# Performance work log

Hardware: AMD Instinct MI355X
Metric: run time of the kernel (lower is better)

## Reference

```python
import jax, jax.numpy as jnp
import numpy as np

B, W, M, HD, RL, RD = 32, 32, 1024, 64, 2, 32
D = RL * HD  # concat of per-layer hidden states


def setup_inputs() -> dict:
    key = jax.random.key(0)
    ks = jax.random.split(key, 16)
    s = 0.1
    r = lambda k, shape: (jax.random.normal(k, shape, jnp.float32) * s)
    return {
        "x_input": jax.random.normal(ks[0], (B, W, M), jnp.float32),
        "major_graph": jax.random.normal(ks[1], (M, M), jnp.float32) * 0.02,
        "H_init": jnp.zeros((RL, M, HD), jnp.float32),
        # GRU layer 0: input size 1 -> hidden HD
        "Wih0": r(ks[2], (3 * HD, 1)),
        "Whh0": r(ks[3], (3 * HD, HD)),
        "bih0": jnp.zeros((3 * HD,), jnp.float32),
        "bhh0": jnp.zeros((3 * HD,), jnp.float32),
        # GRU layer 1: hidden HD -> hidden HD
        "Wih1": r(ks[4], (3 * HD, HD)),
        "Whh1": r(ks[5], (3 * HD, HD)),
        "bih1": jnp.zeros((3 * HD,), jnp.float32),
        "bhh1": jnp.zeros((3 * HD,), jnp.float32),
        # weight-normed Linear(RL*HD -> RD)
        "V": r(ks[6], (RD, D)),
        "g": jnp.ones((RD,), jnp.float32),
        "b_lin": jnp.zeros((RD,), jnp.float32),
        # FinalRowWise layer: per-node weights [M, RD] -> scalar per node
        "W_fr": r(ks[7], (M, RD)),
        "b_fr": jnp.zeros((M,), jnp.float32),
    }


def _gru_cell(x, h, Wih, Whh, bih, bhh):
    # x: [B, M, in], h: [B, M, HD]
    gi = x @ Wih.T + bih
    gh = h @ Whh.T + bhh
    ir, iz, inn = jnp.split(gi, 3, axis=-1)
    hr, hz, hnn = jnp.split(gh, 3, axis=-1)
    rgate = jax.nn.sigmoid(ir + hr)
    zgate = jax.nn.sigmoid(iz + hz)
    n = jnp.tanh(inn + rgate * hnn)
    return (1.0 - zgate) * n + zgate * h


def reference(x_input, major_graph, H_init, Wih0, Whh0, bih0, bhh0,
              Wih1, Whh1, bih1, bhh1, V, g, b_lin, W_fr, b_fr):
    Bn, Wn_, Mn = x_input.shape
    # h0: [RL, B, M, HD] (H_init broadcast over batch)
    h0 = jnp.broadcast_to(H_init[:, None], (H_init.shape[0], Bn, Mn, H_init.shape[-1]))
    # weight_norm (dim=0): per-output-row normalization of V scaled by g
    Wn = g[:, None] * V / jnp.linalg.norm(V, axis=1, keepdims=True)  # [RD, D]
    x_seq = jnp.transpose(x_input, (1, 0, 2))[..., None]  # [W, B, M, 1]

    def step(hn, x_t):
        hn0 = _gru_cell(x_t, hn, Wih0, Whh0, bih0, bhh0)        # [B, M, HD]
        hn1 = _gru_cell(hn0, h0[1], Wih1, Whh1, bih1, bhh1)     # [B, M, HD] (fresh h0 each step, as in source)
        x_p = jnp.concatenate([hn0, hn1], axis=-1)              # [B, M, D]
        # graph-weighted projection along node axis: x_p @ major_graph
        x_g = jax.nn.relu(jnp.einsum('bid,ij->bjd', x_p, major_graph))  # [B, M, D]
        y = jax.nn.sigmoid(x_g @ Wn.T + b_lin)                  # [B, M, RD]
        out = jnp.einsum('bmd,md->bm', y, W_fr) + b_fr          # [B, M]
        return hn1, out

    _, outs = jax.lax.scan(step, h0[0], x_seq)  # [W, B, M]
    return jnp.transpose(outs, (1, 0, 2))       # [B, W, M]
```

## Files before the change

### kernel.cpp

```cpp
#include <hip/hip_runtime.h>
#include <math.h>

#define B_  32
#define W_  32
#define M_  1024
#define HD_ 64
#define RD_ 32
#define D_  128
#define CH_ 16
#define NKT 16

typedef short bf16x8 __attribute__((ext_vector_type(8)));
typedef float f32x4  __attribute__((ext_vector_type(4)));

#define AS1 __attribute__((address_space(1)))
#define AS3 __attribute__((address_space(3)))

__device__ __forceinline__ void gload16(const void* g, void* l) {
    __builtin_amdgcn_global_load_lds((const AS1 void*)g, (AS3 void*)l, 16, 0, 0);
}

__device__ __forceinline__ void bar_lds() {
    asm volatile("s_waitcnt lgkmcnt(0)" ::: "memory");
    __builtin_amdgcn_s_barrier();
    asm volatile("" ::: "memory");
}

__device__ __forceinline__ unsigned short f2b(float f) {
    unsigned int u = __float_as_uint(f);
    u += 0x7fffu + ((u >> 16) & 1u);
    return (unsigned short)(u >> 16);
}
__device__ __forceinline__ float b2f(unsigned short h) {
    return __uint_as_float(((unsigned int)h) << 16);
}
__device__ __forceinline__ float sigf(float x) { return 1.0f / (1.0f + __expf(-x)); }
__device__ __forceinline__ float tanhf_(float x) { return 2.0f / (1.0f + __expf(-2.0f * x)) - 1.0f; }


__global__ __launch_bounds__(256) void gt_kernel(const float* __restrict__ G,
                                                 unsigned short* __restrict__ GTb) {
    __shared__ float T[64][65];
    int i0 = blockIdx.x * 64, j0 = blockIdx.y * 64;
    int tid = threadIdx.x;
    int r = tid >> 4, c4 = (tid & 15) * 4;
    #pragma unroll
    for (int q = 0; q < 4; ++q) {
        float4 v = *(const float4*)&G[(i0 + r + q * 16) * M_ + j0 + c4];
        T[r + q * 16][c4] = v.x; T[r + q * 16][c4 + 1] = v.y;
        T[r + q * 16][c4 + 2] = v.z; T[r + q * 16][c4 + 3] = v.w;
    }
    __syncthreads();
    #pragma unroll
    for (int q = 0; q < 4; ++q) {
        int jr = r + q * 16;
        ushort4 o;
        o.x = f2b(T[c4][jr]); o.y = f2b(T[c4 + 1][jr]);
        o.z = f2b(T[c4 + 2][jr]); o.w = f2b(T[c4 + 3][jr]);
        *(ushort4*)&GTb[(j0 + jr) * M_ + i0 + c4] = o;
    }
}

__global__ __launch_bounds__(192) void gh1ct_kernel(const float* __restrict__ H_init,
                                                    const float* __restrict__ Whh1,
                                                    const float* __restrict__ bhh1,
                                                    float* __restrict__ gh1cT) {
    int m = blockIdx.x, k = threadIdx.x;
    __shared__ float h01[HD_];
    if (k < HD_) h01[k] = H_init[(M_ + m) * HD_ + k];
    __syncthreads();
    float d = 0.f;
    #pragma unroll
    for (int hd = 0; hd < HD_; ++hd) d = fmaf(h01[hd], Whh1[k * HD_ + hd], d);
    gh1cT[k * M_ + m] = d + bhh1[k];
}

__global__ __launch_bounds__(128) void wn_kernel(const float* __restrict__ V,
                                                 const float* __restrict__ g,
                                                 unsigned short* __restrict__ Wnb) {
    int r = blockIdx.x, d = threadIdx.x;
    float v = V[r * D_ + d];
    float s = v * v;
    #pragma unroll
    for (int off = 32; off > 0; off >>= 1) s += __shfl_down(s, off);
    __shared__ float ws[2];
    if ((threadIdx.x & 63) == 0) ws[threadIdx.x >> 6] = s;
    __syncthreads();
    float norm = sqrtf(ws[0] + ws[1]);
    Wnb[r * D_ + d] = f2b(g[r] * v / norm);
}

__global__ __launch_bounds__(256) void castw_kernel(const float* __restrict__ Whh0,
                                                    const float* __restrict__ Wih1,
                                                    unsigned short* __restrict__ Whh0b,
                                                    unsigned short* __restrict__ Wih1b) {
    int i = blockIdx.x * 256 + threadIdx.x;
    Whh0b[i] = f2b(Whh0[i]);
    Wih1b[i] = f2b(Wih1[i]);
}

__global__ __launch_bounds__(256) void inith_kernel(const float* __restrict__ H_init,
                                                    unsigned short* __restrict__ Hb) {
    int e8 = blockIdx.x * 256 + threadIdx.x;
    int base = e8 * 8;
    int src = base & (M_ * HD_ - 1);
    float4 v0 = *(const float4*)&H_init[src];
    float4 v1 = *(const float4*)&H_init[src + 4];
    uint4 u;
    u.x = (unsigned int)f2b(v0.x) | ((unsigned int)f2b(v0.y) << 16);
    u.y = (unsigned int)f2b(v0.z) | ((unsigned int)f2b(v0.w) << 16);
    u.z = (unsigned int)f2b(v1.x) | ((unsigned int)f2b(v1.y) << 16);
    u.w = (unsigned int)f2b(v1.z) | ((unsigned int)f2b(v1.w) << 16);
    *(uint4*)&Hb[base] = u;
}

__global__ __launch_bounds__(512, 4) void gru_chunk_kernel(
    const float* __restrict__ x_input, const float* __restrict__ Wih0,
    const float* __restrict__ bih0, const float* __restrict__ bhh0,
    const unsigned short* __restrict__ Whh0b, const unsigned short* __restrict__ Wih1b,
    const float* __restrict__ bih1, const float* __restrict__ gh1cT,
    const float* __restrict__ H_init, unsigned short* __restrict__ Hb,
    unsigned short* __restrict__ XPT_c, int t0)
{
    __shared__ unsigned short Whh0s[192 * 64];
    __shared__ unsigned short Wih1s[192 * 64];
    __shared__ unsigned short hn0s[64 * 64];
    __shared__ unsigned short hn1s[64 * 64];
    const int tid = threadIdx.x, w = tid >> 6, l = tid & 63;
    const int li = l & 15, lh = l >> 4;
    const int pg = w >> 1, hf = w & 1;
    const int b = blockIdx.x >> 4, mt = blockIdx.x & 15;
    const int m0 = mt * 64;
    const int p0b = b * M_ + m0;
    const int ms = m0 + pg * 16;

    for (int i = tid; i < 1536; i += 512) {
        int row = i >> 3, pos = i & 7, sc = pos ^ (row & 7);
        gload16(&Whh0b[row * 64 + sc * 8], (char*)Whh0s + (i & ~63) * 16);
        gload16(&Wih1b[row * 64 + sc * 8], (char*)Wih1s + (i & ~63) * 16);
    }
    {
        int p = tid >> 3, cc = tid & 7;
        uint4 v = *(const uint4*)&Hb[(p0b + p) * HD_ + cc * 8];
        *(uint4*)((char*)hn1s + p * 128 + ((cc ^ (p & 7)) << 4)) = v;
    }

    float wi_[3][2], bi0_[3][2], bh0_[3][2], bi1_[3][2];
    float vrA[2][4], vzA[2][4], vnA[2][4], h01A[2][4];
    #pragma unroll
    for (int fi = 0; fi < 2; ++fi) {
        int ko = hf * 32 + fi * 16 + li;
        #pragma unroll
        for (int g3 = 0; g3 < 3; ++g3) {
            wi_[g3][fi]  = Wih0[g3 * 64 + ko];
            bi0_[g3][fi] = bih0[g3 * 64 + ko];
            bh0_[g3][fi] = bhh0[g3 * 64 + ko];
            bi1_[g3][fi] = bih1[g3 * 64 + ko];
        }
        float4 vr = *(const float4*)&gh1cT[(ko) * M_ + ms + lh * 4];
        float4 vz = *(const float4*)&gh1cT[(64 + ko) * M_ + ms + lh * 4];
        float4 vn = *(const float4*)&gh1cT[(128 + ko) * M_ + ms + lh * 4];
        vrA[fi][0] = vr.x; vrA[fi][1] = vr.y; vrA[fi][2] = vr.z; vrA[fi][3] = vr.w;
        vzA[fi][0] = vz.x; vzA[fi][1] = vz.y; vzA[fi][2] = vz.z; vzA[fi][3] = vz.w;
        vnA[fi][0] = vn.x; vnA[fi][1] = vn.y; vnA[fi][2] = vn.z; vnA[fi][3] = vn.w;
        #pragma unroll
        for (int reg = 0; reg < 4; ++reg)
            h01A[fi][reg] = H_init[M_ * HD_ + (ms + lh * 4 + reg) * HD_ + ko];
    }

    asm volatile("s_waitcnt vmcnt(0) lgkmcnt(0)" ::: "memory");
    __builtin_amdgcn_s_barrier();
    asm volatile("" ::: "memory");

    float hst[2][4];
    #pragma unroll
    for (int fi = 0; fi < 2; ++fi) {
        int ko = hf * 32 + fi * 16 + li;
        #pragma unroll
        for (int reg = 0; reg < 4; ++reg) {
            int ml = pg * 16 + lh * 4 + reg;
            hst[fi][reg] = b2f(*(const unsigned short*)((char*)hn1s + ml * 128 +
                               ((((ko >> 3) ^ (ml & 7))) << 4) + (ko & 7) * 2));
        }
    }

    for (int ts = 0; ts < CH_; ++ts) {
        int t = t0 + ts;
        float4 xv = *(const float4*)&x_input[(b * W_ + t) * M_ + ms + lh * 4];
        float x4[4] = {xv.x, xv.y, xv.z, xv.w};
        const int rl = pg * 16 + li;

        bf16x8 a0 = *(const bf16x8*)((char*)hn1s + rl * 128 + ((lh ^ (rl & 7)) << 4));
        bf16x8 a1 = *(const bf16x8*)((char*)hn1s + rl * 128 + (((4 + lh) ^ (rl & 7)) << 4));
        f32x4 acc[6];
        #pragma unroll
        for (int q = 0; q < 6; ++q) acc[q] = (f32x4){0.f, 0.f, 0.f, 0.f};
        #pragma unroll
        for (int g3 = 0; g3 < 3; ++g3)
            #pragma unroll
            for (int fi = 0; fi < 2; ++fi) {
                int row = (g3 * 4 + hf * 2 + fi) * 16 + li;
                bf16x8 b0 = *(const bf16x8*)((char*)Whh0s + row * 128 + ((lh ^ (row & 7)) << 4));
                bf16x8 b1 = *(const bf16x8*)((char*)Whh0s + row * 128 + (((4 + lh) ^ (row & 7)) << 4));
                acc[g3 * 2 + fi] = __builtin_amdgcn_mfma_f32_16x16x32_bf16(a0, b0, acc[g3 * 2 + fi], 0, 0, 0);
                acc[g3 * 2 + fi] = __builtin_amdgcn_mfma_f32_16x16x32_bf16(a1, b1, acc[g3 * 2 + fi], 0, 0, 0);
            }
        #pragma unroll
        for (int fi = 0; fi < 2; ++fi) {
            int j = hf * 32 + fi * 16 + li;
            #pragma unroll
            for (int reg = 0; reg < 4; ++reg) {
                int ml = pg * 16 + lh * 4 + reg;
                float x = x4[reg];
                float r = sigf(x * wi_[0][fi] + bi0_[0][fi] + acc[fi][reg]     + bh0_[0][fi]);
                float z = sigf(x * wi_[1][fi] + bi0_[1][fi] + acc[2 + fi][reg] + bh0_[1][fi]);
                float n = tanhf_(x * wi_[2][fi] + bi0_[2][fi] + r * (acc[4 + fi][reg] + bh0_[2][fi]));
                float h0v = (1.f - z) * n + z * hst[fi][reg];
                *(unsigned short*)((char*)hn0s + ml * 128 +
                    ((((j >> 3) ^ (ml & 7))) << 4) + (j & 7) * 2) = f2b(h0v);
            }
        }
        bar_lds();

        a0 = *(const bf16x8*)((char*)hn0s + rl * 128 + ((lh ^ (rl & 7)) << 4));
        a1 = *(const bf16x8*)((char*)hn0s + rl * 128 + (((4 + lh) ^ (rl & 7)) << 4));
        #pragma unroll
        for (int q = 0; q < 6; ++q) acc[q] = (f32x4){0.f, 0.f, 0.f, 0.f};
        #pragma unroll
        for (int g3 = 0; g3 < 3; ++g3)
            #pragma unroll
            for (int fi = 0; fi < 2; ++fi) {
                int row = (g3 * 4 + hf * 2 + fi) * 16 + li;
                bf16x8 b0 = *(const bf16x8*)((char*)Wih1s + row * 128 + ((lh ^ (row & 7)) << 4));
                bf16x8 b1 = *(const bf16x8*)((char*)Wih1s + row * 128 + (((4 + lh) ^ (row & 7)) << 4));
                acc[g3 * 2 + fi] = __builtin_amdgcn_mfma_f32_16x16x32_bf16(a0, b0, acc[g3 * 2 + fi], 0, 0, 0);
                acc[g3 * 2 + fi] = __builtin_amdgcn_mfma_f32_16x16x32_bf16(a1, b1, acc[g3 * 2 + fi], 0, 0, 0);
            }
        #pragma unroll
        for (int fi = 0; fi < 2; ++fi) {
            int ko = hf * 32 + fi * 16 + li;
            #pragma unroll
            for (int reg = 0; reg < 4; ++reg) {
                int ml = pg * 16 + lh * 4 + reg;
                float r = sigf(acc[fi][reg]     + bi1_[0][fi] + vrA[fi][reg]);
                float z = sigf(acc[2 + fi][reg] + bi1_[1][fi] + vzA[fi][reg]);
                float n = tanhf_(acc[4 + fi][reg] + bi1_[2][fi] + r * vnA[fi][reg]);
                float h1v = (1.f - z) * n + z * h01A[fi][reg];
                hst[fi][reg] = h1v;
                *(unsigned short*)((char*)hn1s + ml * 128 +
                    ((((ko >> 3) ^ (ml & 7))) << 4) + (ko & 7) * 2) = f2b(h1v);
            }
        }
        bar_lds();

        {
            unsigned short* XPT = XPT_c + (size_t)ts * (D_ * B_ * M_);
            int d = tid >> 2, mh = (tid & 3) * 16;
            const char* src = (d < 64) ? (const char*)hn0s : (const char*)hn1s;
            int dd = d & 63;
            unsigned int pk[8];
            #pragma unroll
            for (int mm = 0; mm < 16; mm += 2) {
                int ma = mh + mm, mb = mh + mm + 1;
                unsigned int ua = *(const unsigned short*)(src + ma * 128 + (((dd >> 3) ^ (ma & 7)) << 4) + (dd & 7) * 2);
                unsigned int ub = *(const unsigned short*)(src + mb * 128 + (((dd >> 3) ^ (mb & 7)) << 4) + (dd & 7) * 2);
                pk[mm >> 1] = ua | (ub << 16);
            }
            uint4 o0 = {pk[0], pk[1], pk[2], pk[3]};
            uint4 o1 = {pk[4], pk[5], pk[6], pk[7]};
            *(uint4*)&XPT[(b * D_ + d) * M_ + m0 + mh]     = o0;
            *(uint4*)&XPT[(b * D_ + d) * M_ + m0 + mh + 8] = o1;
        }
        bar_lds();
    }

    {
        int p = tid >> 3, cc = tid & 7;
        uint4 v = *(const uint4*)((char*)hn1s + p * 128 + ((cc ^ (p & 7)) << 4));
        *(uint4*)&Hb[(p0b + p) * HD_ + cc * 8] = v;
    }
}

__global__ __launch_bounds__(512, 4) void gemmhead_kernel(
    const unsigned short* __restrict__ GTb, const unsigned short* __restrict__ XPT_c,
    const unsigned short* __restrict__ Wnb, const float* __restrict__ b_lin,
    const float* __restrict__ W_fr, const float* __restrict__ b_fr,
    float* __restrict__ out, int t0)
{
    __shared__ __align__(16) char lds[65536];
    const int tid = threadIdx.x, w = tid >> 6, l = tid & 63;
    const int li = l & 15, lh = l >> 4;
    const int wm = w >> 2, wn = w & 3;
    const int bid = blockIdx.x;
    const int ntile = (bid & 7) + ((bid >> 6) << 3);
    const int j0 = ((bid >> 3) & 7) * 128;
    const unsigned short* Asrc = GTb + (size_t)j0 * M_;
    const unsigned short* Bsrc = XPT_c + (size_t)ntile * 128 * M_;

    f32x4 acc[4][2];
    #pragma unroll
    for (int mi = 0; mi < 4; ++mi)
        #pragma unroll
        for (int ni = 0; ni < 2; ++ni) acc[mi][ni] = (f32x4){0.f, 0.f, 0.f, 0.f};

    #define STAGE(kt, c) { \
        _Pragma("unroll") \
        for (int q = 0; q < 2; ++q) { \
            int i = q * 512 + tid; \
            int row = i >> 3, pos = i & 7, sc = pos ^ (row & 7); \
            gload16(&Asrc[row * M_ + (kt) * 64 + sc * 8], lds + (c) * 32768 + (i & ~63) * 16); \
            gload16(&Bsrc[row * M_ + (kt) * 64 + sc * 8], lds + (c) * 32768 + 16384 + (i & ~63) * 16); \
        } }

    STAGE(0, 0);

    for (int kt = 0; kt < NKT; ++kt) {
        if (kt + 1 < NKT) { STAGE(kt + 1, (kt + 1) & 1);
                            asm volatile("s_waitcnt vmcnt(4)" ::: "memory"); }
        else              { asm volatile("s_waitcnt vmcnt(0)" ::: "memory"); }
        __builtin_amdgcn_s_barrier();
        asm volatile("" ::: "memory");
        const char* Abuf = lds + (kt & 1) * 32768;
        const char* Bbuf = Abuf + 16384;
        bf16x8 af[4][2], bfv[2][2];
        #pragma unroll
        for (int mi = 0; mi < 4; ++mi) {
            int row = wm * 64 + mi * 16 + li;
            #pragma unroll
            for (int kk = 0; kk < 2; ++kk)
                af[mi][kk] = *(const bf16x8*)(Abuf + row * 128 + (((kk * 4 + lh) ^ (row & 7)) << 4));
        }
        #pragma unroll
        for (int ni = 0; ni < 2; ++ni) {
            int row = wn * 32 + ni * 16 + li;
            #pragma unroll
            for (int kk = 0; kk < 2; ++kk)
                bfv[ni][kk] = *(const bf16x8*)(Bbuf + row * 128 + (((kk * 4 + lh) ^ (row & 7)) << 4));
        }
        __builtin_amdgcn_s_setprio(1);
        #pragma unroll
        for (int kk = 0; kk < 2; ++kk)
            #pragma unroll
            for (int mi = 0; mi < 4; ++mi)
                #pragma unroll
                for (int ni = 0; ni < 2; ++ni)
                    acc[mi][ni] = __builtin_amdgcn_mfma_f32_16x16x32_bf16(af[mi][kk], bfv[ni][kk], acc[mi][ni], 0, 0, 0);
        __builtin_amdgcn_s_setprio(0);
        asm volatile("s_waitcnt lgkmcnt(0)" ::: "memory");
        __builtin_amdgcn_s_barrier();
        asm volatile("" ::: "memory");
    }

    __syncthreads();

    #pragma unroll
    for (int mi = 0; mi < 4; ++mi)
        #pragma unroll
        for (int ni = 0; ni < 2; ++ni)
            #pragma unroll
            for (int reg = 0; reg < 4; ++reg) {
                int jl = wm * 64 + mi * 16 + lh * 4 + reg;
                int cl = wn * 32 + ni * 16 + li;
                float v = fmaxf(acc[mi][ni][reg], 0.f);
                int byte = jl * 256 + ((((cl >> 3) ^ (jl & 7))) << 4) + (cl & 7) * 2;
                *(unsigned short*)(lds + byte) = f2b(v);
            }
    __syncthreads();

    const int b = ntile & 31, t = t0 + (ntile >> 5);
    float bl0 = b_lin[li], bl1 = b_lin[16 + li];
    {
        int row = w * 16 + li;
        f32x4 P0 = (f32x4){0.f, 0.f, 0.f, 0.f};
        f32x4 P1 = (f32x4){0.f, 0.f, 0.f, 0.f};
        #pragma unroll
        for (int ks = 0; ks < 4; ++ks) {
            int cp = (ks * 4 + lh) ^ (row & 7);
            bf16x8 xa = *(const bf16x8*)(lds + row * 256 + cp * 16);
            bf16x8 wb0 = *(const bf16x8*)&Wnb[(li) * D_ + ks * 32 + lh * 8];
            bf16x8 wb1 = *(const bf16x8*)&Wnb[(16 + li) * D_ + ks * 32 + lh * 8];
            P0 = __builtin_amdgcn_mfma_f32_16x16x32_bf16(xa, wb0, P0, 0, 0, 0);
            P1 = __builtin_amdgcn_mfma_f32_16x16x32_bf16(xa, wb1, P1, 0, 0, 0);
        }
        float s[4];
        #pragma unroll
        for (int reg = 0; reg < 4; ++reg) {
            int j = j0 + w * 16 + lh * 4 + reg;
            float y0 = sigf(P0[reg] + bl0);
            float y1 = sigf(P1[reg] + bl1);
            s[reg] = y0 * W_fr[j * RD_ + li] + y1 * W_fr[j * RD_ + 16 + li];
        }
        #pragma unroll
        for (int off = 1; off < 16; off <<= 1) {
            #pragma unroll
            for (int reg = 0; reg < 4; ++reg) s[reg] += __shfl_xor(s[reg], off);
        }
        if (li == 0) {
            int jb = j0 + w * 16 + lh * 4;
            float4 o = {s[0] + b_fr[jb], s[1] + b_fr[jb + 1],
                        s[2] + b_fr[jb + 2], s[3] + b_fr[jb + 3]};
            *(float4*)&out[(b * W_ + t) * M_ + jb] = o;
        }
    }
}


extern "C" void kernel_launch(void* const* d_in, const int* in_sizes, int n_in,
                              void* d_out, int out_size, void* d_ws, size_t ws_size,
                              hipStream_t stream) {
    const float* x_input = (const float*)d_in[0];
    const float* G       = (const float*)d_in[1];
    const float* H_init  = (const float*)d_in[2];
    const float* Wih0    = (const float*)d_in[3];
    const float* Whh0    = (const float*)d_in[4];
    const float* bih0    = (const float*)d_in[5];
    const float* bhh0    = (const float*)d_in[6];
    const float* Wih1    = (const float*)d_in[7];
    const float* Whh1    = (const float*)d_in[8];
    const float* bih1    = (const float*)d_in[9];
    const float* bhh1    = (const float*)d_in[10];
    const float* V       = (const float*)d_in[11];
    const float* gvec    = (const float*)d_in[12];
    const float* b_lin   = (const float*)d_in[13];
    const float* W_fr    = (const float*)d_in[14];
    const float* b_fr    = (const float*)d_in[15];
    float* out = (float*)d_out;

    char* ws = (char*)d_ws;
    unsigned short* GTb   = (unsigned short*)(ws);
    unsigned short* XPT_c = (unsigned short*)(ws + (2u   << 20));
    unsigned short* Hb    = (unsigned short*)(ws + (130u << 20));
    float*          gh1cT = (float*)(ws + (134u << 20));
    unsigned short* Wnb   = (unsigned short*)(ws + (135u << 20));
    unsigned short* Whh0b = (unsigned short*)(ws + (135u << 20) + 8192);
    unsigned short* Wih1b = (unsigned short*)(ws + (135u << 20) + 8192 + 24576);

    gt_kernel   <<<dim3(16, 16), 256, 0, stream>>>(G, GTb);
    gh1ct_kernel<<<M_, 192, 0, stream>>>(H_init, Whh1, bhh1, gh1cT);
    wn_kernel   <<<RD_, 128, 0, stream>>>(V, gvec, Wnb);
    castw_kernel<<<48, 256, 0, stream>>>(Whh0, Wih1, Whh0b, Wih1b);
    inith_kernel<<<1024, 256, 0, stream>>>(H_init, Hb);

    for (int c = 0; c < W_ / CH_; ++c) {
        gru_chunk_kernel<<<512, 512, 0, stream>>>(x_input, Wih0, bih0, bhh0, Whh0b,
                                                  Wih1b, bih1, gh1cT, H_init, Hb,
                                                  XPT_c, c * CH_);
        gemmhead_kernel<<<dim3(4096), 512, 0, stream>>>(GTb, XPT_c, Wnb, b_lin,
                                                        W_fr, b_fr, out, c * CH_);
    }
}
```

Before: 584.5 us.

## Double GRU chunk block to 1024 threads, one hidden quarter per wave

```diff
diff --git a/kernel.cpp b/kernel.cpp
--- a/kernel.cpp
+++ b/kernel.cpp
@@ -114,7 +114,7 @@
     *(uint4*)&Hb[base] = u;
 }
 
-__global__ __launch_bounds__(512, 4) void gru_chunk_kernel(
+__global__ __launch_bounds__(1024, 8) void gru_chunk_kernel(
     const float* __restrict__ x_input, const float* __restrict__ Wih0,
     const float* __restrict__ bih0, const float* __restrict__ bhh0,
     const unsigned short* __restrict__ Whh0b, const unsigned short* __restrict__ Wih1b,
@@ -128,60 +128,55 @@
     __shared__ unsigned short hn1s[64 * 64];
     const int tid = threadIdx.x, w = tid >> 6, l = tid & 63;
     const int li = l & 15, lh = l >> 4;
-    const int pg = w >> 1, hf = w & 1;
+    const int pg = w >> 2, qf = w & 3;
     const int b = blockIdx.x >> 4, mt = blockIdx.x & 15;
     const int m0 = mt * 64;
     const int p0b = b * M_ + m0;
     const int ms = m0 + pg * 16;
 
-    for (int i = tid; i < 1536; i += 512) {
+    for (int i = tid; i < 1536; i += 1024) {
         int row = i >> 3, pos = i & 7, sc = pos ^ (row & 7);
         gload16(&Whh0b[row * 64 + sc * 8], (char*)Whh0s + (i & ~63) * 16);
         gload16(&Wih1b[row * 64 + sc * 8], (char*)Wih1s + (i & ~63) * 16);
     }
-    {
+    if (tid < 512) {
         int p = tid >> 3, cc = tid & 7;
         uint4 v = *(const uint4*)&Hb[(p0b + p) * HD_ + cc * 8];
         *(uint4*)((char*)hn1s + p * 128 + ((cc ^ (p & 7)) << 4)) = v;
     }
 
-    float wi_[3][2], bi0_[3][2], bh0_[3][2], bi1_[3][2];
-    float vrA[2][4], vzA[2][4], vnA[2][4], h01A[2][4];
-    #pragma unroll
-    for (int fi = 0; fi < 2; ++fi) {
-        int ko = hf * 32 + fi * 16 + li;
-        #pragma unroll
-        for (int g3 = 0; g3 < 3; ++g3) {
-            wi_[g3][fi]  = Wih0[g3 * 64 + ko];
-            bi0_[g3][fi] = bih0[g3 * 64 + ko];
-            bh0_[g3][fi] = bhh0[g3 * 64 + ko];
-            bi1_[g3][fi] = bih1[g3 * 64 + ko];
-        }
+    const int ko = qf * 16 + li;
+    float wi_[3], bi0_[3], bh0_[3], bi1_[3];
+    #pragma unroll
+    for (int g3 = 0; g3 < 3; ++g3) {
+        wi_[g3]  = Wih0[g3 * 64 + ko];
+        bi0_[g3] = bih0[g3 * 64 + ko];
+        bh0_[g3] = bhh0[g3 * 64 + ko];
+        bi1_[g3] = bih1[g3 * 64 + ko];
+    }
+    float vrA[4], vzA[4], vnA[4], h01A[4];
+    {
         float4 vr = *(const float4*)&gh1cT[(ko) * M_ + ms + lh * 4];
         float4 vz = *(const float4*)&gh1cT[(64 + ko) * M_ + ms + lh * 4];
         float4 vn = *(const float4*)&gh1cT[(128 + ko) * M_ + ms + lh * 4];
-        vrA[fi][0] = vr.x; vrA[fi][1] = vr.y; vrA[fi][2] = vr.z; vrA[fi][3] = vr.w;
-        vzA[fi][0] = vz.x; vzA[fi][1] = vz.y; vzA[fi][2] = vz.z; vzA[fi][3] = vz.w;
-        vnA[fi][0] = vn.x; vnA[fi][1] = vn.y; vnA[fi][2] = vn.z; vnA[fi][3] = vn.w;
+        vrA[0] = vr.x; vrA[1] = vr.y; vrA[2] = vr.z; vrA[3] = vr.w;
+        vzA[0] = vz.x; vzA[1] = vz.y; vzA[2] = vz.z; vzA[3] = vz.w;
+        vnA[0] = vn.x; vnA[1] = vn.y; vnA[2] = vn.z; vnA[3] = vn.w;
         #pragma unroll
         for (int reg = 0; reg < 4; ++reg)
-            h01A[fi][reg] = H_init[M_ * HD_ + (ms + lh * 4 + reg) * HD_ + ko];
+            h01A[reg] = H_init[M_ * HD_ + (ms + lh * 4 + reg) * HD_ + ko];
     }
 
     asm volatile("s_waitcnt vmcnt(0) lgkmcnt(0)" ::: "memory");
     __builtin_amdgcn_s_barrier();
     asm volatile("" ::: "memory");
 
-    float hst[2][4];
-    #pragma unroll
-    for (int fi = 0; fi < 2; ++fi) {
-        int ko = hf * 32 + fi * 16 + li;
-        #pragma unroll
-        for (int reg = 0; reg < 4; ++reg) {
-            int ml = pg * 16 + lh * 4 + reg;
-            hst[fi][reg] = b2f(*(const unsigned short*)((char*)hn1s + ml * 128 +
-                               ((((ko >> 3) ^ (ml & 7))) << 4) + (ko & 7) * 2));
-        }
+    float hst[4];
+    #pragma unroll
+    for (int reg = 0; reg < 4; ++reg) {
+        int ml = pg * 16 + lh * 4 + reg;
+        hst[reg] = b2f(*(const unsigned short*)((char*)hn1s + ml * 128 +
+                       ((((ko >> 3) ^ (ml & 7))) << 4) + (ko & 7) * 2));
     }
 
     for (int ts = 0; ts < CH_; ++ts) {
@@ -192,89 +187,75 @@
 
         bf16x8 a0 = *(const bf16x8*)((char*)hn1s + rl * 128 + ((lh ^ (rl & 7)) << 4));
         bf16x8 a1 = *(const bf16x8*)((char*)hn1s + rl * 128 + (((4 + lh) ^ (rl & 7)) << 4));
-        f32x4 acc[6];
-        #pragma unroll
-        for (int q = 0; q < 6; ++q) acc[q] = (f32x4){0.f, 0.f, 0.f, 0.f};
-        #pragma unroll
-        for (int g3 = 0; g3 < 3; ++g3)
-            #pragma unroll
-            for (int fi = 0; fi < 2; ++fi) {
-                int row = (g3 * 4 + hf * 2 + fi) * 16 + li;
-                bf16x8 b0 = *(const bf16x8*)((char*)Whh0s + row * 128 + ((lh ^ (row & 7)) << 4));
-                bf16x8 b1 = *(const bf16x8*)((char*)Whh0s + row * 128 + (((4 + lh) ^ (row & 7)) << 4));
-                acc[g3 * 2 + fi] = __builtin_amdgcn_mfma_f32_16x16x32_bf16(a0, b0, acc[g3 * 2 + fi], 0, 0, 0);
-                acc[g3 * 2 + fi] = __builtin_amdgcn_mfma_f32_16x16x32_bf16(a1, b1, acc[g3 * 2 + fi], 0, 0, 0);
-            }
-        #pragma unroll
-        for (int fi = 0; fi < 2; ++fi) {
-            int j = hf * 32 + fi * 16 + li;
-            #pragma unroll
-            for (int reg = 0; reg < 4; ++reg) {
-                int ml = pg * 16 + lh * 4 + reg;
-                float x = x4[reg];
-                float r = sigf(x * wi_[0][fi] + bi0_[0][fi] + acc[fi][reg]     + bh0_[0][fi]);
-                float z = sigf(x * wi_[1][fi] + bi0_[1][fi] + acc[2 + fi][reg] + bh0_[1][fi]);
-                float n = tanhf_(x * wi_[2][fi] + bi0_[2][fi] + r * (acc[4 + fi][reg] + bh0_[2][fi]));
-                float h0v = (1.f - z) * n + z * hst[fi][reg];
-                *(unsigned short*)((char*)hn0s + ml * 128 +
-                    ((((j >> 3) ^ (ml & 7))) << 4) + (j & 7) * 2) = f2b(h0v);
-            }
+        f32x4 acc[3];
+        #pragma unroll
+        for (int q = 0; q < 3; ++q) acc[q] = (f32x4){0.f, 0.f, 0.f, 0.f};
+        #pragma unroll
+        for (int g3 = 0; g3 < 3; ++g3) {
+            int row = (g3 * 4 + qf) * 16 + li;
+            bf16x8 b0 = *(const bf16x8*)((char*)Whh0s + row * 128 + ((lh ^ (row & 7)) << 4));
+            bf16x8 b1 = *(const bf16x8*)((char*)Whh0s + row * 128 + (((4 + lh) ^ (row & 7)) << 4));
+            acc[g3] = __builtin_amdgcn_mfma_f32_16x16x32_bf16(a0, b0, acc[g3], 0, 0, 0);
+            acc[g3] = __builtin_amdgcn_mfma_f32_16x16x32_bf16(a1, b1, acc[g3], 0, 0, 0);
+        }
+        #pragma unroll
+        for (int reg = 0; reg < 4; ++reg) {
+            int ml = pg * 16 + lh * 4 + reg;
+            float x = x4[reg];
+            float r = sigf(x * wi_[0] + bi0_[0] + acc[0][reg] + bh0_[0]);
+            float z = sigf(x * wi_[1] + bi0_[1] + acc[1][reg] + bh0_[1]);
+            float n = tanhf_(x * wi_[2] + bi0_[2] + r * (acc[2][reg] + bh0_[2]));
+            float h0v = (1.f - z) * n + z * hst[reg];
+            *(unsigned short*)((char*)hn0s + ml * 128 +
+                ((((ko >> 3) ^ (ml & 7))) << 4) + (ko & 7) * 2) = f2b(h0v);
         }
         bar_lds();
 
         a0 = *(const bf16x8*)((char*)hn0s + rl * 128 + ((lh ^ (rl & 7)) << 4));
         a1 = *(const bf16x8*)((char*)hn0s + rl * 128 + (((4 + lh) ^ (rl & 7)) << 4));
         #pragma unroll
-        for (int q = 0; q < 6; ++q) acc[q] = (f32x4){0.f, 0.f, 0.f, 0.f};
-        #pragma unroll
-        for (int g3 = 0; g3 < 3; ++g3)
-            #pragma unroll
-            for (int fi = 0; fi < 2; ++fi) {
-                int row = (g3 * 4 + hf * 2 + fi) * 16 + li;
-                bf16x8 b0 = *(const bf16x8*)((char*)Wih1s + row * 128 + ((lh ^ (row & 7)) << 4));
-                bf16x8 b1 = *(const bf16x8*)((char*)Wih1s + row * 128 + (((4 + lh) ^ (row & 7)) << 4));
-                acc[g3 * 2 + fi] = __builtin_amdgcn_mfma_f32_16x16x32_bf16(a0, b0, acc[g3 * 2 + fi], 0, 0, 0);
-                acc[g3 * 2 + fi] = __builtin_amdgcn_mfma_f32_16x16x32_bf16(a1, b1, acc[g3 * 2 + fi], 0, 0, 0);
-            }
-        #pragma unroll
-        for (int fi = 0; fi < 2; ++fi) {
-            int ko = hf * 32 + fi * 16 + li;
-            #pragma unroll
-            for (int reg = 0; reg < 4; ++reg) {
-                int ml = pg * 16 + lh * 4 + reg;
-                float r = sigf(acc[fi][reg]     + bi1_[0][fi] + vrA[fi][reg]);
-                float z = sigf(acc[2 + fi][reg] + bi1_[1][fi] + vzA[fi][reg]);
-                float n = tanhf_(acc[4 + fi][reg] + bi1_[2][fi] + r * vnA[fi][reg]);
-                float h1v = (1.f - z) * n + z * h01A[fi][reg];
-                hst[fi][reg] = h1v;
-                *(unsigned short*)((char*)hn1s + ml * 128 +
-                    ((((ko >> 3) ^ (ml & 7))) << 4) + (ko & 7) * 2) = f2b(h1v);
-            }
+        for (int q = 0; q < 3; ++q) acc[q] = (f32x4){0.f, 0.f, 0.f, 0.f};
+        #pragma unroll
+        for (int g3 = 0; g3 < 3; ++g3) {
+            int row = (g3 * 4 + qf) * 16 + li;
+            bf16x8 b0 = *(const bf16x8*)((char*)Wih1s + row * 128 + ((lh ^ (row & 7)) << 4));
+            bf16x8 b1 = *(const bf16x8*)((char*)Wih1s + row * 128 + (((4 + lh) ^ (row & 7)) << 4));
+            acc[g3] = __builtin_amdgcn_mfma_f32_16x16x32_bf16(a0, b0, acc[g3], 0, 0, 0);
+            acc[g3] = __builtin_amdgcn_mfma_f32_16x16x32_bf16(a1, b1, acc[g3], 0, 0, 0);
+        }
+        #pragma unroll
+        for (int reg = 0; reg < 4; ++reg) {
+            int ml = pg * 16 + lh * 4 + reg;
+            float r = sigf(acc[0][reg] + bi1_[0] + vrA[reg]);
+            float z = sigf(acc[1][reg] + bi1_[1] + vzA[reg]);
+            float n = tanhf_(acc[2][reg] + bi1_[2] + r * vnA[reg]);
+            float h1v = (1.f - z) * n + z * h01A[reg];
+            hst[reg] = h1v;
+            *(unsigned short*)((char*)hn1s + ml * 128 +
+                ((((ko >> 3) ^ (ml & 7))) << 4) + (ko & 7) * 2) = f2b(h1v);
         }
         bar_lds();
 
         {
             unsigned short* XPT = XPT_c + (size_t)ts * (D_ * B_ * M_);
-            int d = tid >> 2, mh = (tid & 3) * 16;
+            int d = tid >> 3, mh = (tid & 7) * 8;
             const char* src = (d < 64) ? (const char*)hn0s : (const char*)hn1s;
             int dd = d & 63;
-            unsigned int pk[8];
-            #pragma unroll
-            for (int mm = 0; mm < 16; mm += 2) {
+            unsigned int pk[4];
+            #pragma unroll
+            for (int mm = 0; mm < 8; mm += 2) {
                 int ma = mh + mm, mb = mh + mm + 1;
                 unsigned int ua = *(const unsigned short*)(src + ma * 128 + (((dd >> 3) ^ (ma & 7)) << 4) + (dd & 7) * 2);
                 unsigned int ub = *(const unsigned short*)(src + mb * 128 + (((dd >> 3) ^ (mb & 7)) << 4) + (dd & 7) * 2);
                 pk[mm >> 1] = ua | (ub << 16);
             }
             uint4 o0 = {pk[0], pk[1], pk[2], pk[3]};
-            uint4 o1 = {pk[4], pk[5], pk[6], pk[7]};
-            *(uint4*)&XPT[(b * D_ + d) * M_ + m0 + mh]     = o0;
-            *(uint4*)&XPT[(b * D_ + d) * M_ + m0 + mh + 8] = o1;
+            *(uint4*)&XPT[(b * D_ + d) * M_ + m0 + mh] = o0;
         }
         bar_lds();
     }
 
-    {
+    if (tid < 512) {
         int p = tid >> 3, cc = tid & 7;
         uint4 v = *(const uint4*)((char*)hn1s + p * 128 + ((cc ^ (p & 7)) << 4));
         *(uint4*)&Hb[(p0b + p) * HD_ + cc * 8] = v;
@@ -442,9 +423,9 @@
     inith_kernel<<<1024, 256, 0, stream>>>(H_init, Hb);
 
     for (int c = 0; c < W_ / CH_; ++c) {
-        gru_chunk_kernel<<<512, 512, 0, stream>>>(x_input, Wih0, bih0, bhh0, Whh0b,
-                                                  Wih1b, bih1, gh1cT, H_init, Hb,
-                                                  XPT_c, c * CH_);
+        gru_chunk_kernel<<<512, 1024, 0, stream>>>(x_input, Wih0, bih0, bhh0, Whh0b,
+                                                   Wih1b, bih1, gh1cT, H_init, Hb,
+                                                   XPT_c, c * CH_);
         gemmhead_kernel<<<dim3(4096), 512, 0, stream>>>(GTb, XPT_c, Wnb, b_lin,
                                                         W_fr, b_fr, out, c * CH_);
     }
```

New measurement: 642.1 us. 1.1x slower.
